# Optimization experiments

Hardware: AMD Instinct MI355X
Metric: run time of the kernel (lower is better)

The kernel has to match this reference:

```python
import jax, jax.numpy as jnp
import numpy as np

B, D, C = 16384, 1024, 2048

def setup_inputs() -> dict:
    key = jax.random.key(0)
    k1, k2 = jax.random.split(key)
    x = jax.random.normal(k1, (B, D), dtype=jnp.float32)
    # kaiming_normal_ with nonlinearity='relu': std = sqrt(2 / fan_in)
    W = jax.random.normal(k2, (C, D), dtype=jnp.float32) * jnp.sqrt(2.0 / D)
    return {"x": x, "W": W, "task_id": 0}

def reference(x, W, task_id):
    # Original: -(x[:, :, None] - W.T[None, :, :])**2 .mean(1)  -> [B, C]
    # Algebraic rewrite: -(||x||^2/D - 2*x.W^T/D + ||w||^2/D)
    d = jnp.asarray(x.shape[1], x.dtype)
    x2 = jnp.sum(x * x, axis=1, keepdims=True) / d          # [B, 1]
    w2 = jnp.sum(W * W, axis=1) / d                          # [C]
    cross = jnp.einsum('bd,cd->bc', x, W) * (2.0 / d)        # [B, C]
    return cross - x2 - w2[None, :]
```

## Files before the change

kernel.cpp:

```cpp
#include <hip/hip_runtime.h>
#include <hip/hip_bf16.h>
#include <stdint.h>

#define B_ROWS 16384
#define D_DIM  1024
#define C_DIM  2048
#define MT_TOT (B_ROWS / 16)
#define NT_TOT (C_DIM  / 16)
#define KT_TOT (D_DIM  / 32)

typedef short bf16x8 __attribute__((ext_vector_type(8)));
typedef float f32x4  __attribute__((ext_vector_type(4)));

__global__ __launch_bounds__(256) void pack_norm(
        const float* __restrict__ x, const float* __restrict__ W,
        ushort* __restrict__ Apk, ushort* __restrict__ Bpk,
        float* __restrict__ x2, float* __restrict__ w2) {
    int chunk = blockIdx.x * 4 + (threadIdx.x >> 6);
    const int lane = threadIdx.x & 63;
    const int XCH = MT_TOT * KT_TOT;
    const float* src; ushort* dst; float* norm;
    if (chunk < XCH) { src = x; dst = Apk; norm = x2; }
    else             { src = W; dst = Bpk; norm = w2; chunk -= XCH; }
    const int tile = chunk >> 5;
    const int kt   = chunk & 31;

    const int row = tile * 16 + (lane & 15);
    const int k0  = kt * 32 + (lane >> 4) * 8;
    const float4 v0 = *(const float4*)(src + (size_t)row * D_DIM + k0);
    const float4 v1 = *(const float4*)(src + (size_t)row * D_DIM + k0 + 4);
    float s = v0.x*v0.x + v0.y*v0.y + v0.z*v0.z + v0.w*v0.w
            + v1.x*v1.x + v1.y*v1.y + v1.z*v1.z + v1.w*v1.w;

    ushort u[8]; __hip_bfloat16 h;
    h = __float2bfloat16(v0.x); u[0] = *(const ushort*)&h;
    h = __float2bfloat16(v0.y); u[1] = *(const ushort*)&h;
    h = __float2bfloat16(v0.z); u[2] = *(const ushort*)&h;
    h = __float2bfloat16(v0.w); u[3] = *(const ushort*)&h;
    h = __float2bfloat16(v1.x); u[4] = *(const ushort*)&h;
    h = __float2bfloat16(v1.y); u[5] = *(const ushort*)&h;
    h = __float2bfloat16(v1.z); u[6] = *(const ushort*)&h;
    h = __float2bfloat16(v1.w); u[7] = *(const ushort*)&h;
    *(bf16x8*)(dst + ((size_t)chunk * 64 + lane) * 8) = *(const bf16x8*)u;

    s += __shfl_xor(s, 16, 64);
    s += __shfl_xor(s, 32, 64);
    if (lane < 16) atomicAdd(norm + tile * 16 + lane, s * (1.0f / (float)D_DIM));
}

__global__ __launch_bounds__(256, 3) void gemm_flat(
        const ushort* __restrict__ Apk, const ushort* __restrict__ Bpk,
        const float* __restrict__ x2, const float* __restrict__ w2,
        float* __restrict__ out) {
    const int tid  = threadIdx.x;
    const int lane = tid & 63;
    const int wv   = tid >> 6;

    const int wid = (blockIdx.x & 7) * 256 + (blockIdx.x >> 3);
    const int bm  = wid >> 4;
    const int bn  = wid & 15;
    const int mT0 = bm * 8 + (wv >> 1) * 4;
    const int nT0 = bn * 8 + (wv & 1) * 4;

    const ushort* aP = Apk + ((size_t)mT0 * KT_TOT) * 512 + lane * 8;
    const ushort* bP = Bpk + ((size_t)nT0 * KT_TOT) * 512 + lane * 8;

    f32x4 acc[4][4];
    #pragma unroll
    for (int mi = 0; mi < 4; ++mi)
        #pragma unroll
        for (int ni = 0; ni < 4; ++ni)
            acc[mi][ni] = (f32x4){0.f, 0.f, 0.f, 0.f};

    bf16x8 aC[4], bC[4], aN[4], bN[4];

    #pragma unroll
    for (int i = 0; i < 4; ++i) {
        aC[i] = *(const bf16x8*)(aP + i * (KT_TOT * 512));
        bC[i] = *(const bf16x8*)(bP + i * (KT_TOT * 512));
    }

    #pragma unroll 4
    for (int kt = 0; kt < KT_TOT; kt += 2) {
        const int k1 = kt + 1;
        const int k2 = (kt + 2 < KT_TOT) ? kt + 2 : KT_TOT - 1;
        #pragma unroll
        for (int i = 0; i < 4; ++i) {
            aN[i] = *(const bf16x8*)(aP + i * (KT_TOT * 512) + k1 * 512);
            bN[i] = *(const bf16x8*)(bP + i * (KT_TOT * 512) + k1 * 512);
        }
        #pragma unroll
        for (int mi = 0; mi < 4; ++mi)
            #pragma unroll
            for (int ni = 0; ni < 4; ++ni)
                acc[mi][ni] = __builtin_amdgcn_mfma_f32_16x16x32_bf16(
                    aC[mi], bC[ni], acc[mi][ni], 0, 0, 0);
        #pragma unroll
        for (int i = 0; i < 4; ++i) {
            aC[i] = *(const bf16x8*)(aP + i * (KT_TOT * 512) + k2 * 512);
            bC[i] = *(const bf16x8*)(bP + i * (KT_TOT * 512) + k2 * 512);
        }
        #pragma unroll
        for (int mi = 0; mi < 4; ++mi)
            #pragma unroll
            for (int ni = 0; ni < 4; ++ni)
                acc[mi][ni] = __builtin_amdgcn_mfma_f32_16x16x32_bf16(
                    aN[mi], bN[ni], acc[mi][ni], 0, 0, 0);
    }

    const float scale = 2.0f / (float)D_DIM;
    const int rsel = lane & 15;
    const int quad = lane >> 4;
    const int row0 = mT0 * 16 + quad * 4;
    const int col0 = nT0 * 16 + rsel;

    float x2r[4][4];
    #pragma unroll
    for (int mi = 0; mi < 4; ++mi)
        #pragma unroll
        for (int r = 0; r < 4; ++r)
            x2r[mi][r] = x2[row0 + mi * 16 + r];

    #pragma unroll
    for (int ni = 0; ni < 4; ++ni) {
        const int c = col0 + ni * 16;
        const float wc = w2[c];
        #pragma unroll
        for (int mi = 0; mi < 4; ++mi) {
            #pragma unroll
            for (int r = 0; r < 4; ++r) {
                const int rr = row0 + mi * 16 + r;
                out[(size_t)rr * C_DIM + c] = acc[mi][ni][r] * scale - x2r[mi][r] - wc;
            }
        }
    }
}

extern "C" void kernel_launch(void* const* d_in, const int* in_sizes, int n_in,
                              void* d_out, int out_size, void* d_ws, size_t ws_size,
                              hipStream_t stream) {
    const float* x = (const float*)d_in[0];
    const float* W = (const float*)d_in[1];
    float* out = (float*)d_out;

    char* ws = (char*)d_ws;
    ushort* Apk = (ushort*)ws;
    ushort* Bpk = (ushort*)(ws + (size_t)B_ROWS * D_DIM * sizeof(ushort));
    float*  x2  = (float*)(ws + (size_t)(B_ROWS + C_DIM) * D_DIM * sizeof(ushort));
    float*  w2  = x2 + B_ROWS;

    hipMemsetAsync(x2, 0, (B_ROWS + C_DIM) * sizeof(float), stream);

    pack_norm<<<(MT_TOT * KT_TOT + NT_TOT * KT_TOT) / 4, 256, 0, stream>>>(
        x, W, Apk, Bpk, x2, w2);

    gemm_flat<<<(B_ROWS / 128) * (C_DIM / 128), 256, 0, stream>>>(
        Apk, Bpk, x2, w2, out);
}
```

Measured before the change: 301.2 us.

## Stage packed A/B tiles in LDS via direct global-to-LDS loads

Replaces the per-wave direct global register loads with block-cooperative staging. Each block loads its packed A and B k-slices into shared memory with global_load_lds, and waves then read their fragments from LDS. Each global fragment is fetched once per block instead of twice, since two waves share each A or B tile. The cost is two barriers per two k-steps and no double buffering, so global loads no longer overlap the MFMA work.

```diff
diff --git a/kernel.cpp b/kernel.cpp
--- a/kernel.cpp
+++ b/kernel.cpp
@@ -48,10 +48,13 @@
     if (lane < 16) atomicAdd(norm + tile * 16 + lane, s * (1.0f / (float)D_DIM));
 }
 
-__global__ __launch_bounds__(256, 3) void gemm_flat(
+__global__ __launch_bounds__(256, 3) void gemm_pklds(
         const ushort* __restrict__ Apk, const ushort* __restrict__ Bpk,
         const float* __restrict__ x2, const float* __restrict__ w2,
         float* __restrict__ out) {
+    __shared__ ushort As[16 * 512];
+    __shared__ ushort Bs[16 * 512];
+
     const int tid  = threadIdx.x;
     const int lane = tid & 63;
     const int wv   = tid >> 6;
@@ -59,11 +62,12 @@
     const int wid = (blockIdx.x & 7) * 256 + (blockIdx.x >> 3);
     const int bm  = wid >> 4;
     const int bn  = wid & 15;
-    const int mT0 = bm * 8 + (wv >> 1) * 4;
-    const int nT0 = bn * 8 + (wv & 1) * 4;
 
-    const ushort* aP = Apk + ((size_t)mT0 * KT_TOT) * 512 + lane * 8;
-    const ushort* bP = Bpk + ((size_t)nT0 * KT_TOT) * 512 + lane * 8;
+    const ushort* aSrc = Apk + ((size_t)(bm * 8) * KT_TOT) * 512 + lane * 8;
+    const ushort* bSrc = Bpk + ((size_t)(bn * 8) * KT_TOT) * 512 + lane * 8;
+
+    const ushort* aRd = As + (wv >> 1) * 4 * 1024 + lane * 8;
+    const ushort* bRd = Bs + (wv & 1) * 4 * 1024 + lane * 8;
 
     f32x4 acc[4][4];
     #pragma unroll
@@ -72,45 +76,54 @@
         for (int ni = 0; ni < 4; ++ni)
             acc[mi][ni] = (f32x4){0.f, 0.f, 0.f, 0.f};
 
-    bf16x8 aC[4], bC[4], aN[4], bN[4];
+    for (int kt = 0; kt < KT_TOT; kt += 2) {
+        if (wv < 2) {
+            #pragma unroll
+            for (int r = 0; r < 8; ++r) {
+                const int c    = wv * 8 + r;
+                const int tile = c >> 1, ks = c & 1;
+                __builtin_amdgcn_global_load_lds(
+                    (const __attribute__((address_space(1))) void*)(
+                        aSrc + ((size_t)tile * KT_TOT + kt + ks) * 512),
+                    (__attribute__((address_space(3))) void*)(As + c * 512), 16, 0, 0);
+            }
+        } else {
+            #pragma unroll
+            for (int r = 0; r < 8; ++r) {
+                const int c    = (wv - 2) * 8 + r;
+                const int tile = c >> 1, ks = c & 1;
+                __builtin_amdgcn_global_load_lds(
+                    (const __attribute__((address_space(1))) void*)(
+                        bSrc + ((size_t)tile * KT_TOT + kt + ks) * 512),
+                    (__attribute__((address_space(3))) void*)(Bs + c * 512), 16, 0, 0);
+            }
+        }
+        __syncthreads();
 
-    #pragma unroll
-    for (int i = 0; i < 4; ++i) {
-        aC[i] = *(const bf16x8*)(aP + i * (KT_TOT * 512));
-        bC[i] = *(const bf16x8*)(bP + i * (KT_TOT * 512));
-    }
-
-    #pragma unroll 4
-    for (int kt = 0; kt < KT_TOT; kt += 2) {
-        const int k1 = kt + 1;
-        const int k2 = (kt + 2 < KT_TOT) ? kt + 2 : KT_TOT - 1;
         #pragma unroll
-        for (int i = 0; i < 4; ++i) {
-            aN[i] = *(const bf16x8*)(aP + i * (KT_TOT * 512) + k1 * 512);
-            bN[i] = *(const bf16x8*)(bP + i * (KT_TOT * 512) + k1 * 512);
-        }
-        #pragma unroll
-        for (int mi = 0; mi < 4; ++mi)
+        for (int ks = 0; ks < 2; ++ks) {
+            bf16x8 a[4], b[4];
+            #pragma unroll
+            for (int mi = 0; mi < 4; ++mi)
+                a[mi] = *(const bf16x8*)(aRd + mi * 1024 + ks * 512);
             #pragma unroll
             for (int ni = 0; ni < 4; ++ni)
-                acc[mi][ni] = __builtin_amdgcn_mfma_f32_16x16x32_bf16(
-                    aC[mi], bC[ni], acc[mi][ni], 0, 0, 0);
-        #pragma unroll
-        for (int i = 0; i < 4; ++i) {
-            aC[i] = *(const bf16x8*)(aP + i * (KT_TOT * 512) + k2 * 512);
-            bC[i] = *(const bf16x8*)(bP + i * (KT_TOT * 512) + k2 * 512);
+                b[ni] = *(const bf16x8*)(bRd + ni * 1024 + ks * 512);
+            #pragma unroll
+            for (int mi = 0; mi < 4; ++mi)
+                #pragma unroll
+                for (int ni = 0; ni < 4; ++ni)
+                    acc[mi][ni] = __builtin_amdgcn_mfma_f32_16x16x32_bf16(
+                        a[mi], b[ni], acc[mi][ni], 0, 0, 0);
         }
-        #pragma unroll
-        for (int mi = 0; mi < 4; ++mi)
-            #pragma unroll
-            for (int ni = 0; ni < 4; ++ni)
-                acc[mi][ni] = __builtin_amdgcn_mfma_f32_16x16x32_bf16(
-                    aN[mi], bN[ni], acc[mi][ni], 0, 0, 0);
+        __syncthreads();
     }
 
     const float scale = 2.0f / (float)D_DIM;
     const int rsel = lane & 15;
     const int quad = lane >> 4;
+    const int mT0  = bm * 8 + (wv >> 1) * 4;
+    const int nT0  = bn * 8 + (wv & 1) * 4;
     const int row0 = mT0 * 16 + quad * 4;
     const int col0 = nT0 * 16 + rsel;
 
@@ -154,6 +167,6 @@
     pack_norm<<<(MT_TOT * KT_TOT + NT_TOT * KT_TOT) / 4, 256, 0, stream>>>(
         x, W, Apk, Bpk, x2, w2);
 
-    gemm_flat<<<(B_ROWS / 128) * (C_DIM / 128), 256, 0, stream>>>(
+    gemm_pklds<<<(B_ROWS / 128) * (C_DIM / 128), 256, 0, stream>>>(
         Apk, Bpk, x2, w2, out);
 }
```

Result: faster. 251.8 us (-16.4%).
